# Kernel optimization log

Measured on AMD Instinct MI355X. Metric: run time of the kernel, lower is better.

The kernel has to match this reference:

```python
import jax, jax.numpy as jnp
import numpy as np

EPS_NORM = 1e-12  # F.normalize eps
EPS_BN = 1e-5     # BatchNorm eps


def setup_inputs() -> dict:
    key = jax.random.key(0)
    ks = jax.random.split(key, 8)
    B, N, P, d = 64, 4, 128, 256  # batch, subgraphs, patches/subgraph, feature_dim
    h = 256                        # hidden2[-1]
    C = 2                          # num_class
    totP = N * P                   # 512 == num_patches
    feat = totP * h                # readout size = 131072

    def w(k, shape, s=0.02):
        return jax.random.normal(k, shape, dtype=jnp.float32) * s

    return {
        "x": jax.random.normal(ks[0], (B, totP, d), dtype=jnp.float32),
        "edge_prior_mask": jax.random.uniform(ks[1], (P, P), dtype=jnp.float32),
        # stage1 GCN layers (Linear stored as [in, out])
        "W1": w(ks[2], (d, h)), "b1": jnp.zeros((h,), jnp.float32),
        "g1": jnp.ones((h,), jnp.float32), "be1": jnp.zeros((h,), jnp.float32),
        "W2": w(ks[3], (h, h)), "b2": jnp.zeros((h,), jnp.float32),
        "g2": jnp.ones((h,), jnp.float32), "be2": jnp.zeros((h,), jnp.float32),
        # mlp_causal
        "Wm1": w(ks[4], (feat, 128), 0.005), "bm1": jnp.zeros((128,), jnp.float32),
        "gm1": jnp.ones((128,), jnp.float32), "bem1": jnp.zeros((128,), jnp.float32),
        "Wm2": w(ks[5], (128, 64)), "bm2": jnp.zeros((64,), jnp.float32),
        "gm2": jnp.ones((64,), jnp.float32), "bem2": jnp.zeros((64,), jnp.float32),
        "Wm3": w(ks[6], (64, C)), "bm3": jnp.zeros((C,), jnp.float32),
    }


def reference(x, edge_prior_mask, W1, b1, g1, be1, W2, b2, g2, be2,
              Wm1, bm1, gm1, bem1, Wm2, bm2, gm2, bem2, Wm3, bm3):
    B, totP, d = x.shape
    P = edge_prior_mask.shape[0]
    N = totP // P

    # ---- dynamic edges: per-subgraph cosine similarity * prior mask ----
    xb = x.reshape(B, N, P, d)
    nrm = jnp.linalg.norm(xb, axis=-1, keepdims=True)
    xn = xb / jnp.maximum(nrm, EPS_NORM)
    sim = (jnp.einsum('bnpd,bnqd->bnpq', xn, xn) + 1.0) * 0.5  # [B,N,P,P]
    blocks = sim * edge_prior_mask[None, None]

    # block-diagonal assembly [B, totP, totP]
    edges = jnp.zeros((B, totP, totP), dtype=x.dtype)
    for i in range(N):
        edges = edges.at[:, i * P:(i + 1) * P, i * P:(i + 1) * P].set(blocks[:, i])
    eye = jnp.eye(totP, dtype=x.dtype)
    edges = edges * (1.0 - eye)  # zero the diagonal

    # ---- symmetric degree normalization with self loops ----
    A = edges + eye
    deg = A.sum(-1)  # [B, totP]
    dinv = jnp.where(deg > 0, 1.0 / jnp.sqrt(jnp.maximum(deg, EPS_NORM)), 0.0)
    An = dinv[:, :, None] * A * dinv[:, None, :]

    # ---- two GCN layers: bmm(An, X @ W + b) -> BN (over batch+nodes) -> relu ----
    def bn_relu(hh, g, b):
        m = hh.mean(axis=(0, 1), keepdims=True)
        v = hh.var(axis=(0, 1), keepdims=True)
        return jax.nn.relu(g * (hh - m) / jnp.sqrt(v + EPS_BN) + b)

    h1 = bn_relu(jnp.einsum('bpq,bqh->bph', An, x @ W1 + b1), g1, be1)
    h2 = bn_relu(jnp.einsum('bpq,bqh->bph', An, h1 @ W2 + b2), g2, be2)

    # ---- readout + MLP head (dropout = identity in eval) ----
    graph = h2.reshape(B, -1)

    def bn1d(z, g, b):
        m = z.mean(0, keepdims=True)
        v = z.var(0, keepdims=True)
        return g * (z - m) / jnp.sqrt(v + EPS_BN) + b

    z = jax.nn.relu(bn1d(graph @ Wm1 + bm1, gm1, bem1))
    z = jax.nn.relu(bn1d(z @ Wm2 + bm2, gm2, bem2))
    return z @ Wm3 + bm3
```

## Files before the change

### kernel.cpp

```cpp
#include <hip/hip_runtime.h>
#include <cstdint>
#include <cstddef>

#define P_    128
#define H_    256
#define FEAT_ 131072

__global__ __launch_bounds__(256) void k_simfused(
    const float* __restrict__ x, const float* __restrict__ mask,
    float* __restrict__ An) {
  __shared__ float Xs[16][128];
  __shared__ float red[128][17];
  __shared__ float diag_s[128];
  __shared__ float inv_s[128];
  __shared__ float dinv_s[128];
  const int blk = blockIdx.x;
  const int t = threadIdx.x;
  const int tp = t >> 4, tq = t & 15;
  const float* Xb = x + (size_t)blk * (128 * 256);

  float v[8][8];
  #pragma unroll
  for (int i = 0; i < 8; ++i)
    #pragma unroll
    for (int j = 0; j < 8; ++j) v[i][j] = 0.f;

  for (int kc = 0; kc < 16; ++kc) {
    __syncthreads();
    #pragma unroll
    for (int l = 0; l < 2; ++l) {
      const int f = t + 256 * l;
      const int row = f >> 2, k4 = (f & 3) * 4;
      const float4 x4 = *(const float4*)(Xb + (size_t)row * 256 + kc * 16 + k4);
      Xs[k4 + 0][row] = x4.x;
      Xs[k4 + 1][row] = x4.y;
      Xs[k4 + 2][row] = x4.z;
      Xs[k4 + 3][row] = x4.w;
    }
    __syncthreads();
    #pragma unroll
    for (int k = 0; k < 16; ++k) {
      const float4 a0 = *(const float4*)&Xs[k][tp * 8];
      const float4 a1 = *(const float4*)&Xs[k][tp * 8 + 4];
      const float4 b0 = *(const float4*)&Xs[k][tq * 8];
      const float4 b1 = *(const float4*)&Xs[k][tq * 8 + 4];
      const float a[8] = {a0.x, a0.y, a0.z, a0.w, a1.x, a1.y, a1.z, a1.w};
      const float b[8] = {b0.x, b0.y, b0.z, b0.w, b1.x, b1.y, b1.z, b1.w};
      #pragma unroll
      for (int i = 0; i < 8; ++i)
        #pragma unroll
        for (int j = 0; j < 8; ++j) v[i][j] += a[i] * b[j];
    }
  }

  if (tp == tq) {
    #pragma unroll
    for (int i = 0; i < 8; ++i) diag_s[tp * 8 + i] = v[i][i];
  }
  __syncthreads();
  if (t < 128) inv_s[t] = 1.0f / fmaxf(sqrtf(diag_s[t]), 1e-12f);
  __syncthreads();

  float ivq[8];
  #pragma unroll
  for (int j = 0; j < 8; ++j) ivq[j] = inv_s[tq * 8 + j];

  #pragma unroll
  for (int i = 0; i < 8; ++i) {
    const int r = tp * 8 + i;
    const float ivp = inv_s[r];
    const float4 m0 = *(const float4*)(mask + r * 128 + tq * 8);
    const float4 m1 = *(const float4*)(mask + r * 128 + tq * 8 + 4);
    const float mm[8] = {m0.x, m0.y, m0.z, m0.w, m1.x, m1.y, m1.z, m1.w};
    float s = 0.f;
    #pragma unroll
    for (int j = 0; j < 8; ++j) {
      const int c = tq * 8 + j;
      const float vv = (r == c) ? 0.0f
                                : (v[i][j] * ivp * ivq[j] + 1.0f) * 0.5f * mm[j];
      v[i][j] = vv;
      s += vv;
    }
    red[r][tq] = s;
  }
  __syncthreads();
  if (t < 128) {
    float sm = 0.f;
    #pragma unroll
    for (int u = 0; u < 16; ++u) sm += red[t][u];
    const float deg = 1.0f + sm;
    dinv_s[t] = (deg > 0.0f) ? rsqrtf(fmaxf(deg, 1e-12f)) : 0.0f;
  }
  __syncthreads();

  float dq[8];
  #pragma unroll
  for (int j = 0; j < 8; ++j) dq[j] = dinv_s[tq * 8 + j];
  float* Ab = An + (size_t)blk * 16384;
  #pragma unroll
  for (int i = 0; i < 8; ++i) {
    const int r = tp * 8 + i;
    const float dp = dinv_s[r];
    float o[8];
    #pragma unroll
    for (int j = 0; j < 8; ++j) {
      const int c = tq * 8 + j;
      o[j] = (r == c) ? dp * dq[j] : v[i][j] * dp * dq[j];
    }
    *(float4*)(Ab + (size_t)r * 128 + tq * 8)     = make_float4(o[0], o[1], o[2], o[3]);
    *(float4*)(Ab + (size_t)r * 128 + tq * 8 + 4) = make_float4(o[4], o[5], o[6], o[7]);
  }
}

__global__ __launch_bounds__(256) void k_gemm_t(
    const float* __restrict__ A, const float* __restrict__ W,
    const float* __restrict__ bias, float* __restrict__ out) {
  __shared__ float As[16][132];
  __shared__ float Ws[16][132];
  const int rb = blockIdx.x, cb = blockIdx.y;
  const int t = threadIdx.x, tp = t >> 4, tq = t & 15;
  const int m0 = rb * 128, c0 = cb * 128;

  float acc[8][8];
  #pragma unroll
  for (int j = 0; j < 8; ++j) {
    const int cj = (j < 4) ? (tq * 4 + j) : (64 + tq * 4 + (j - 4));
    const float bj = bias[c0 + cj];
    #pragma unroll
    for (int i = 0; i < 8; ++i) acc[i][j] = bj;
  }

  for (int kc = 0; kc < 16; ++kc) {
    __syncthreads();
    #pragma unroll
    for (int l = 0; l < 2; ++l) {
      const int f = t + 256 * l;
      const int row = f >> 2, k4 = (f & 3) * 4;
      const float4 a4 = *(const float4*)(A + (size_t)(m0 + row) * 256 + kc * 16 + k4);
      As[k4 + 0][row] = a4.x;
      As[k4 + 1][row] = a4.y;
      As[k4 + 2][row] = a4.z;
      As[k4 + 3][row] = a4.w;
    }
    #pragma unroll
    for (int l = 0; l < 2; ++l) {
      const int f = t + 256 * l;
      const int k = f >> 5, c4 = (f & 31) * 4;
      *(float4*)&Ws[k][c4] =
          *(const float4*)(W + (size_t)(kc * 16 + k) * 256 + c0 + c4);
    }
    __syncthreads();
    #pragma unroll
    for (int k = 0; k < 16; ++k) {
      const float4 a0 = *(const float4*)&As[k][tp * 4];
      const float4 a1 = *(const float4*)&As[k][64 + tp * 4];
      const float4 w0 = *(const float4*)&Ws[k][tq * 4];
      const float4 w1 = *(const float4*)&Ws[k][64 + tq * 4];
      const float a[8] = {a0.x, a0.y, a0.z, a0.w, a1.x, a1.y, a1.z, a1.w};
      const float w[8] = {w0.x, w0.y, w0.z, w0.w, w1.x, w1.y, w1.z, w1.w};
      #pragma unroll
      for (int i = 0; i < 8; ++i)
        #pragma unroll
        for (int j = 0; j < 8; ++j) acc[i][j] += a[i] * w[j];
    }
  }

  #pragma unroll
  for (int i = 0; i < 8; ++i) {
    const int ri = (i < 4) ? (tp * 4 + i) : (64 + tp * 4 + (i - 4));
    float* orow = out + (size_t)(m0 + ri) * 256 + c0;
    *(float4*)(orow + tq * 4)      = make_float4(acc[i][0], acc[i][1], acc[i][2], acc[i][3]);
    *(float4*)(orow + 64 + tq * 4) = make_float4(acc[i][4], acc[i][5], acc[i][6], acc[i][7]);
  }
}

__global__ __launch_bounds__(256) void k_gemmbn_t(
    const float* __restrict__ A, const float* __restrict__ scsh,
    const float* __restrict__ W, const float* __restrict__ bias,
    float* __restrict__ out) {
  __shared__ float As[16][132];
  __shared__ float Ws[16][132];
  const int rb = blockIdx.x, cb = blockIdx.y;
  const int t = threadIdx.x, tp = t >> 4, tq = t & 15;
  const int m0 = rb * 128, c0 = cb * 128;

  float acc[8][8];
  #pragma unroll
  for (int j = 0; j < 8; ++j) {
    const int cj = (j < 4) ? (tq * 4 + j) : (64 + tq * 4 + (j - 4));
    const float bj = bias[c0 + cj];
    #pragma unroll
    for (int i = 0; i < 8; ++i) acc[i][j] = bj;
  }

  for (int kc = 0; kc < 16; ++kc) {
    __syncthreads();
    #pragma unroll
    for (int l = 0; l < 2; ++l) {
      const int f = t + 256 * l;
      const int row = f >> 2, k4 = (f & 3) * 4;
      const int col = kc * 16 + k4;
      const float4 a4 = *(const float4*)(A + (size_t)(m0 + row) * 256 + col);
      const float4 sc = *(const float4*)(scsh + col);
      const float4 sh = *(const float4*)(scsh + 256 + col);
      As[k4 + 0][row] = fmaxf(a4.x * sc.x + sh.x, 0.0f);
      As[k4 + 1][row] = fmaxf(a4.y * sc.y + sh.y, 0.0f);
      As[k4 + 2][row] = fmaxf(a4.z * sc.z + sh.z, 0.0f);
      As[k4 + 3][row] = fmaxf(a4.w * sc.w + sh.w, 0.0f);
    }
    #pragma unroll
    for (int l = 0; l < 2; ++l) {
      const int f = t + 256 * l;
      const int k = f >> 5, c4 = (f & 31) * 4;
      *(float4*)&Ws[k][c4] =
          *(const float4*)(W + (size_t)(kc * 16 + k) * 256 + c0 + c4);
    }
    __syncthreads();
    #pragma unroll
    for (int k = 0; k < 16; ++k) {
      const float4 a0 = *(const float4*)&As[k][tp * 4];
      const float4 a1 = *(const float4*)&As[k][64 + tp * 4];
      const float4 w0 = *(const float4*)&Ws[k][tq * 4];
      const float4 w1 = *(const float4*)&Ws[k][64 + tq * 4];
      const float a[8] = {a0.x, a0.y, a0.z, a0.w, a1.x, a1.y, a1.z, a1.w};
      const float w[8] = {w0.x, w0.y, w0.z, w0.w, w1.x, w1.y, w1.z, w1.w};
      #pragma unroll
      for (int i = 0; i < 8; ++i)
        #pragma unroll
        for (int j = 0; j < 8; ++j) acc[i][j] += a[i] * w[j];
    }
  }

  #pragma unroll
  for (int i = 0; i < 8; ++i) {
    const int ri = (i < 4) ? (tp * 4 + i) : (64 + tp * 4 + (i - 4));
    float* orow = out + (size_t)(m0 + ri) * 256 + c0;
    *(float4*)(orow + tq * 4)      = make_float4(acc[i][0], acc[i][1], acc[i][2], acc[i][3]);
    *(float4*)(orow + 64 + tq * 4) = make_float4(acc[i][4], acc[i][5], acc[i][6], acc[i][7]);
  }
}

__global__ __launch_bounds__(256) void k_bmmst(
    const float* __restrict__ An, const float* __restrict__ XW,
    float* __restrict__ out, float* __restrict__ part) {
  __shared__ float As[16][132];
  __shared__ float Ws[16][132];
  __shared__ float rs[16][128];
  __shared__ float rq[16][128];
  const int blk = blockIdx.x, cb = blockIdx.y;
  const int t = threadIdx.x, tp = t >> 4, tq = t & 15;
  const float* Ab = An + (size_t)blk * 16384;
  const float* Xb = XW + (size_t)blk * (128 * 256);

  float acc[8][8];
  #pragma unroll
  for (int i = 0; i < 8; ++i)
    #pragma unroll
    for (int j = 0; j < 8; ++j) acc[i][j] = 0.f;

  for (int kc = 0; kc < 8; ++kc) {
    __syncthreads();
    #pragma unroll
    for (int l = 0; l < 2; ++l) {
      const int f = t + 256 * l;
      const int row = f >> 2, k4 = (f & 3) * 4;
      const float4 a4 = *(const float4*)(Ab + (size_t)row * 128 + kc * 16 + k4);
      As[k4 + 0][row] = a4.x;
      As[k4 + 1][row] = a4.y;
      As[k4 + 2][row] = a4.z;
      As[k4 + 3][row] = a4.w;
    }
    #pragma unroll
    for (int l = 0; l < 2; ++l) {
      const int f = t + 256 * l;
      const int k = f >> 5, c4 = (f & 31) * 4;
      *(float4*)&Ws[k][c4] =
          *(const float4*)(Xb + (size_t)(kc * 16 + k) * 256 + cb * 128 + c4);
    }
    __syncthreads();
    #pragma unroll
    for (int k = 0; k < 16; ++k) {
      const float4 a0 = *(const float4*)&As[k][tp * 4];
      const float4 a1 = *(const float4*)&As[k][64 + tp * 4];
      const float4 w0 = *(const float4*)&Ws[k][tq * 4];
      const float4 w1 = *(const float4*)&Ws[k][64 + tq * 4];
      const float a[8] = {a0.x, a0.y, a0.z, a0.w, a1.x, a1.y, a1.z, a1.w};
      const float w[8] = {w0.x, w0.y, w0.z, w0.w, w1.x, w1.y, w1.z, w1.w};
      #pragma unroll
      for (int i = 0; i < 8; ++i)
        #pragma unroll
        for (int j = 0; j < 8; ++j) acc[i][j] += a[i] * w[j];
    }
  }

  #pragma unroll
  for (int j = 0; j < 8; ++j) {
    const int col = (j < 4) ? (tq * 4 + j) : (64 + tq * 4 + (j - 4));
    float cs = 0.f, cq = 0.f;
    #pragma unroll
    for (int i = 0; i < 8; ++i) { cs += acc[i][j]; cq += acc[i][j] * acc[i][j]; }
    rs[tp][col] = cs;
    rq[tp][col] = cq;
  }
  __syncthreads();
  if (t < 128) {
    float s = 0.f, q = 0.f;
    #pragma unroll
    for (int u = 0; u < 16; ++u) { s += rs[u][t]; q += rq[u][t]; }
    const int base = (blk * 2 + cb) * 256;
    part[base + t]       = s;
    part[base + 128 + t] = q;
  }

  #pragma unroll
  for (int i = 0; i < 8; ++i) {
    const int ri = (i < 4) ? (tp * 4 + i) : (64 + tp * 4 + (i - 4));
    float* orow = out + (size_t)(blk * 128 + ri) * 256 + cb * 128;
    *(float4*)(orow + tq * 4)      = make_float4(acc[i][0], acc[i][1], acc[i][2], acc[i][3]);
    *(float4*)(orow + 64 + tq * 4) = make_float4(acc[i][4], acc[i][5], acc[i][6], acc[i][7]);
  }
}

__global__ __launch_bounds__(256) void k_bnscsh(
    const float* __restrict__ part, const float* __restrict__ g,
    const float* __restrict__ be, float* __restrict__ scsh) {
  __shared__ float ss[256], qq[256];
  const int c = blockIdx.x;
  const int cb = c >> 7, lc = c & 127;
  const int u = threadIdx.x;
  const float* pb = part + (size_t)(u * 2 + cb) * 256;
  ss[u] = pb[lc];
  qq[u] = pb[128 + lc];
  __syncthreads();
  for (int st = 128; st; st >>= 1) {
    if (u < st) { ss[u] += ss[u + st]; qq[u] += qq[u + st]; }
    __syncthreads();
  }
  if (u == 0) {
    const float m = ss[0] * (1.0f / 32768.0f);
    const float var = qq[0] * (1.0f / 32768.0f) - m * m;
    const float sc = g[c] * rsqrtf(var + 1e-5f);
    scsh[c] = sc;
    scsh[256 + c] = be[c] - m * sc;
  }
}

__global__ __launch_bounds__(256) void k_headgemm_v3(
    const float* __restrict__ pre2, const float* __restrict__ scsh,
    const float* __restrict__ Wm1, float* __restrict__ part) {
  __shared__ float graphS[64][128];
  const int t = threadIdx.x;
  const int bid = blockIdx.x;
  const int k0 = bid * 128;
  const int cbase = k0 & 255;

  #pragma unroll
  for (int l = 0; l < 8; ++l) {
    const int f = t + 256 * l;
    const int row = f >> 5, c4 = (f & 31) * 4;
    const float4 p = *(const float4*)(pre2 + (size_t)row * FEAT_ + k0 + c4);
    const float4 sc = *(const float4*)(scsh + cbase + c4);
    const float4 sh = *(const float4*)(scsh + 256 + cbase + c4);
    graphS[row][c4 + 0] = fmaxf(p.x * sc.x + sh.x, 0.0f);
    graphS[row][c4 + 1] = fmaxf(p.y * sc.y + sh.y, 0.0f);
    graphS[row][c4 + 2] = fmaxf(p.z * sc.z + sh.z, 0.0f);
    graphS[row][c4 + 3] = fmaxf(p.w * sc.w + sh.w, 0.0f);
  }
  __syncthreads();

  const int hg = t & 31;
  const int bg = t >> 5;
  float acc[8][4];
  #pragma unroll
  for (int i = 0; i < 8; ++i)
    #pragma unroll
    for (int j = 0; j < 4; ++j) acc[i][j] = 0.f;

  #pragma unroll 2
  for (int kk = 0; kk < 128; kk += 4) {
    const int k = k0 + kk;
    const float4 w0 = *(const float4*)(Wm1 + (size_t)(k + 0) * 128 + hg * 4);
    const float4 w1 = *(const float4*)(Wm1 + (size_t)(k + 1) * 128 + hg * 4);
    const float4 w2 = *(const float4*)(Wm1 + (size_t)(k + 2) * 128 + hg * 4);
    const float4 w3 = *(const float4*)(Wm1 + (size_t)(k + 3) * 128 + hg * 4);
    #pragma unroll
    for (int i = 0; i < 8; ++i) {
      const float4 a = *(const float4*)&graphS[bg * 8 + i][kk];
      acc[i][0] += a.x * w0.x; acc[i][1] += a.x * w0.y;
      acc[i][2] += a.x * w0.z; acc[i][3] += a.x * w0.w;
      acc[i][0] += a.y * w1.x; acc[i][1] += a.y * w1.y;
      acc[i][2] += a.y * w1.z; acc[i][3] += a.y * w1.w;
      acc[i][0] += a.z * w2.x; acc[i][1] += a.z * w2.y;
      acc[i][2] += a.z * w2.z; acc[i][3] += a.z * w2.w;
      acc[i][0] += a.w * w3.x; acc[i][1] += a.w * w3.y;
      acc[i][2] += a.w * w3.z; acc[i][3] += a.w * w3.w;
    }
  }

  float* pb = part + (size_t)bid * 8192;
  #pragma unroll
  for (int i = 0; i < 8; ++i)
    *(float4*)(pb + (bg * 8 + i) * 128 + hg * 4) =
        make_float4(acc[i][0], acc[i][1], acc[i][2], acc[i][3]);
}

__global__ __launch_bounds__(256) void k_headredA(
    const float* __restrict__ part, float* __restrict__ part2) {
  const int o = blockIdx.x * 256 + threadIdx.x;
  const int jg = blockIdx.y;
  const float* base = part + (size_t)jg * 128 * 8192;
  float s = 0.f;
  for (int j = 0; j < 128; ++j) s += base[(size_t)j * 8192 + o];
  part2[(size_t)jg * 8192 + o] = s;
}

__global__ __launch_bounds__(256) void k_headtail(
    const float* __restrict__ part2,
    const float* __restrict__ gm1, const float* __restrict__ bem1,
    const float* __restrict__ Wm2,
    const float* __restrict__ gm2, const float* __restrict__ bem2,
    const float* __restrict__ Wm3, const float* __restrict__ bm3,
    float* __restrict__ out) {
  __shared__ float zs[8192];
  __shared__ float wm2s[8192];
  __shared__ float zb2[4096];
  __shared__ float sc1[128], sh1[128], sc2[64], sh2[64];
  const int t = threadIdx.x;

  for (int o = t; o < 8192; o += 256) {
    float s = 0.f;
    #pragma unroll
    for (int jg = 0; jg < 8; ++jg) s += part2[(size_t)jg * 8192 + o];
    zs[o] = s;
  }
  for (int o = t; o < 8192; o += 256) wm2s[o] = Wm2[o];
  __syncthreads();

  if (t < 128) {
    float s = 0.f, q = 0.f;
    for (int b = 0; b < 64; ++b) { const float v = zs[b * 128 + t]; s += v; q += v * v; }
    const float m = s * (1.0f / 64.0f);
    const float var = q * (1.0f / 64.0f) - m * m;
    const float sc = gm1[t] * rsqrtf(var + 1e-5f);
    sc1[t] = sc; sh1[t] = bem1[t] - m * sc;
  }
  __syncthreads();
  for (int o = t; o < 8192; o += 256)
    zs[o] = fmaxf(zs[o] * sc1[o & 127] + sh1[o & 127], 0.0f);
  __syncthreads();

  {
    const int bq = t >> 4, jq = t & 15;
    float acc[4][4];
    #pragma unroll
    for (int bi = 0; bi < 4; ++bi)
      #pragma unroll
      for (int ji = 0; ji < 4; ++ji) acc[bi][ji] = 0.f;
    for (int k = 0; k < 128; ++k) {
      const float4 w4 = *(const float4*)&wm2s[k * 64 + jq * 4];
      const float wv[4] = {w4.x, w4.y, w4.z, w4.w};
      #pragma unroll
      for (int bi = 0; bi < 4; ++bi) {
        const float zv = zs[(bq * 4 + bi) * 128 + k];
        #pragma unroll
        for (int ji = 0; ji < 4; ++ji) acc[bi][ji] += zv * wv[ji];
      }
    }
    #pragma unroll
    for (int bi = 0; bi < 4; ++bi)
      #pragma unroll
      for (int ji = 0; ji < 4; ++ji)
        zb2[(bq * 4 + bi) * 64 + jq * 4 + ji] = acc[bi][ji];
  }
  __syncthreads();

  if (t < 64) {
    float s = 0.f, q = 0.f;
    for (int b = 0; b < 64; ++b) { const float v = zb2[b * 64 + t]; s += v; q += v * v; }
    const float m = s * (1.0f / 64.0f);
    const float var = q * (1.0f / 64.0f) - m * m;
    const float sc = gm2[t] * rsqrtf(var + 1e-5f);
    sc2[t] = sc; sh2[t] = bem2[t] - m * sc;
  }
  __syncthreads();
  for (int idx = t; idx < 4096; idx += 256)
    zb2[idx] = fmaxf(zb2[idx] * sc2[idx & 63] + sh2[idx & 63], 0.0f);
  __syncthreads();

  if (t < 128) {
    const int b = t >> 1, c = t & 1;
    float s = bm3[c];
    for (int k = 0; k < 64; ++k) s += zb2[b * 64 + k] * Wm3[k * 2 + c];
    out[t] = s;
  }
}

extern "C" void kernel_launch(void* const* d_in, const int* in_sizes, int n_in,
                              void* d_out, int out_size, void* d_ws, size_t ws_size,
                              hipStream_t stream) {
  (void)in_sizes; (void)n_in; (void)out_size; (void)ws_size;
  const float* x    = (const float*)d_in[0];
  const float* mask = (const float*)d_in[1];
  const float* W1   = (const float*)d_in[2];
  const float* b1   = (const float*)d_in[3];
  const float* g1   = (const float*)d_in[4];
  const float* be1  = (const float*)d_in[5];
  const float* W2   = (const float*)d_in[6];
  const float* b2   = (const float*)d_in[7];
  const float* g2   = (const float*)d_in[8];
  const float* be2  = (const float*)d_in[9];
  const float* Wm1  = (const float*)d_in[10];
  const float* gm1  = (const float*)d_in[12];
  const float* bem1 = (const float*)d_in[13];
  const float* Wm2  = (const float*)d_in[14];
  const float* gm2  = (const float*)d_in[16];
  const float* bem2 = (const float*)d_in[17];
  const float* Wm3  = (const float*)d_in[18];
  const float* bm3  = (const float*)d_in[19];

  float* ws   = (float*)d_ws;
  float* T1   = ws;
  float* An   = T1 + 8388608;
  float* T2   = An + 4194304;
  float* T3   = T2 + 8388608;
  float* z1   = T3 + 8388608;
  float* dinv = z1 + 8192;
  (void)z1;

  float* scsh1 = dinv;
  float* scsh2 = dinv + 512;

  k_simfused<<<256, 256, 0, stream>>>(x, mask, An);

  k_gemm_t<<<dim3(256, 2), 256, 0, stream>>>(x, W1, b1, T2);
  k_bmmst<<<dim3(256, 2), 256, 0, stream>>>(An, T2, T3, T1);
  k_bnscsh<<<256, 256, 0, stream>>>(T1, g1, be1, scsh1);

  k_gemmbn_t<<<dim3(256, 2), 256, 0, stream>>>(T3, scsh1, W2, b2, T2);
  k_bmmst<<<dim3(256, 2), 256, 0, stream>>>(An, T2, T3, T1);
  k_bnscsh<<<256, 256, 0, stream>>>(T1, g2, be2, scsh2);

  k_headgemm_v3<<<1024, 256, 0, stream>>>(T3, scsh2, Wm1, T2);
  k_headredA<<<dim3(32, 8), 256, 0, stream>>>(T2, An);
  k_headtail<<<1, 256, 0, stream>>>(An, gm1, bem1, Wm2, gm2, bem2,
                                    Wm3, bm3, (float*)d_out);
}
```

Measured before the change: 412.5 us.

## Split-K the first feature GEMM and double threads in similarity kernel

The first X@W1 GEMM is split into two K halves across a third grid dimension. Each half writes its own partial buffer, and the following batched An@XW kernel adds the two partials while loading its tile. The similarity/adjacency kernel now uses 512 threads per block, each computing 4x8 outputs instead of 8x8, to raise occupancy on a grid with only 256 blocks. The cost is an extra 32 MB partial write and read, plus a dropped restrict qualifier because the bmm input aliases its output buffer.

```diff
diff --git a/kernel.cpp b/kernel.cpp
--- a/kernel.cpp
+++ b/kernel.cpp
@@ -6,7 +6,7 @@
 #define H_    256
 #define FEAT_ 131072
 
-__global__ __launch_bounds__(256) void k_simfused(
+__global__ __launch_bounds__(512) void k_simfused(
     const float* __restrict__ x, const float* __restrict__ mask,
     float* __restrict__ An) {
   __shared__ float Xs[16][128];
@@ -19,18 +19,16 @@
   const int tp = t >> 4, tq = t & 15;
   const float* Xb = x + (size_t)blk * (128 * 256);
 
-  float v[8][8];
-  #pragma unroll
-  for (int i = 0; i < 8; ++i)
+  float v[4][8];
+  #pragma unroll
+  for (int i = 0; i < 4; ++i)
     #pragma unroll
     for (int j = 0; j < 8; ++j) v[i][j] = 0.f;
 
   for (int kc = 0; kc < 16; ++kc) {
     __syncthreads();
-    #pragma unroll
-    for (int l = 0; l < 2; ++l) {
-      const int f = t + 256 * l;
-      const int row = f >> 2, k4 = (f & 3) * 4;
+    {
+      const int row = t >> 2, k4 = (t & 3) * 4;
       const float4 x4 = *(const float4*)(Xb + (size_t)row * 256 + kc * 16 + k4);
       Xs[k4 + 0][row] = x4.x;
       Xs[k4 + 1][row] = x4.y;
@@ -40,22 +38,23 @@
     __syncthreads();
     #pragma unroll
     for (int k = 0; k < 16; ++k) {
-      const float4 a0 = *(const float4*)&Xs[k][tp * 8];
-      const float4 a1 = *(const float4*)&Xs[k][tp * 8 + 4];
+      const float4 a0 = *(const float4*)&Xs[k][tp * 4];
       const float4 b0 = *(const float4*)&Xs[k][tq * 8];
       const float4 b1 = *(const float4*)&Xs[k][tq * 8 + 4];
-      const float a[8] = {a0.x, a0.y, a0.z, a0.w, a1.x, a1.y, a1.z, a1.w};
+      const float a[4] = {a0.x, a0.y, a0.z, a0.w};
       const float b[8] = {b0.x, b0.y, b0.z, b0.w, b1.x, b1.y, b1.z, b1.w};
       #pragma unroll
-      for (int i = 0; i < 8; ++i)
+      for (int i = 0; i < 4; ++i)
         #pragma unroll
         for (int j = 0; j < 8; ++j) v[i][j] += a[i] * b[j];
     }
   }
 
-  if (tp == tq) {
-    #pragma unroll
-    for (int i = 0; i < 8; ++i) diag_s[tp * 8 + i] = v[i][i];
+  #pragma unroll
+  for (int i = 0; i < 4; ++i) {
+    const int r = tp * 4 + i;
+    const int jd = r - tq * 8;
+    if (jd >= 0 && jd < 8) diag_s[r] = v[i][jd];
   }
   __syncthreads();
   if (t < 128) inv_s[t] = 1.0f / fmaxf(sqrtf(diag_s[t]), 1e-12f);
@@ -66,8 +65,8 @@
   for (int j = 0; j < 8; ++j) ivq[j] = inv_s[tq * 8 + j];
 
   #pragma unroll
-  for (int i = 0; i < 8; ++i) {
-    const int r = tp * 8 + i;
+  for (int i = 0; i < 4; ++i) {
+    const int r = tp * 4 + i;
     const float ivp = inv_s[r];
     const float4 m0 = *(const float4*)(mask + r * 128 + tq * 8);
     const float4 m1 = *(const float4*)(mask + r * 128 + tq * 8 + 4);
@@ -98,8 +97,8 @@
   for (int j = 0; j < 8; ++j) dq[j] = dinv_s[tq * 8 + j];
   float* Ab = An + (size_t)blk * 16384;
   #pragma unroll
-  for (int i = 0; i < 8; ++i) {
-    const int r = tp * 8 + i;
+  for (int i = 0; i < 4; ++i) {
+    const int r = tp * 4 + i;
     const float dp = dinv_s[r];
     float o[8];
     #pragma unroll
@@ -114,29 +113,31 @@
 
 __global__ __launch_bounds__(256) void k_gemm_t(
     const float* __restrict__ A, const float* __restrict__ W,
-    const float* __restrict__ bias, float* __restrict__ out) {
+    const float* __restrict__ bias, float* __restrict__ out0,
+    float* __restrict__ out1) {
   __shared__ float As[16][132];
   __shared__ float Ws[16][132];
-  const int rb = blockIdx.x, cb = blockIdx.y;
+  const int rb = blockIdx.x, cb = blockIdx.y, kh = blockIdx.z;
   const int t = threadIdx.x, tp = t >> 4, tq = t & 15;
-  const int m0 = rb * 128, c0 = cb * 128;
+  const int m0 = rb * 128, c0 = cb * 128, kbase = kh * 128;
 
   float acc[8][8];
   #pragma unroll
   for (int j = 0; j < 8; ++j) {
     const int cj = (j < 4) ? (tq * 4 + j) : (64 + tq * 4 + (j - 4));
-    const float bj = bias[c0 + cj];
+    const float bj = (kh == 0) ? bias[c0 + cj] : 0.0f;
     #pragma unroll
     for (int i = 0; i < 8; ++i) acc[i][j] = bj;
   }
 
-  for (int kc = 0; kc < 16; ++kc) {
+  for (int kc = 0; kc < 8; ++kc) {
     __syncthreads();
     #pragma unroll
     for (int l = 0; l < 2; ++l) {
       const int f = t + 256 * l;
       const int row = f >> 2, k4 = (f & 3) * 4;
-      const float4 a4 = *(const float4*)(A + (size_t)(m0 + row) * 256 + kc * 16 + k4);
+      const float4 a4 = *(const float4*)(A + (size_t)(m0 + row) * 256 +
+                                         kbase + kc * 16 + k4);
       As[k4 + 0][row] = a4.x;
       As[k4 + 1][row] = a4.y;
       As[k4 + 2][row] = a4.z;
@@ -147,7 +148,7 @@
       const int f = t + 256 * l;
       const int k = f >> 5, c4 = (f & 31) * 4;
       *(float4*)&Ws[k][c4] =
-          *(const float4*)(W + (size_t)(kc * 16 + k) * 256 + c0 + c4);
+          *(const float4*)(W + (size_t)(kbase + kc * 16 + k) * 256 + c0 + c4);
     }
     __syncthreads();
     #pragma unroll
@@ -165,10 +166,11 @@
     }
   }
 
+  float* outp = kh ? out1 : out0;
   #pragma unroll
   for (int i = 0; i < 8; ++i) {
     const int ri = (i < 4) ? (tp * 4 + i) : (64 + tp * 4 + (i - 4));
-    float* orow = out + (size_t)(m0 + ri) * 256 + c0;
+    float* orow = outp + (size_t)(m0 + ri) * 256 + c0;
     *(float4*)(orow + tq * 4)      = make_float4(acc[i][0], acc[i][1], acc[i][2], acc[i][3]);
     *(float4*)(orow + 64 + tq * 4) = make_float4(acc[i][4], acc[i][5], acc[i][6], acc[i][7]);
   }
@@ -241,8 +243,8 @@
 }
 
 __global__ __launch_bounds__(256) void k_bmmst(
-    const float* __restrict__ An, const float* __restrict__ XW,
-    float* __restrict__ out, float* __restrict__ part) {
+    const float* __restrict__ An, const float* XW0, const float* XW1,
+    float* out, float* __restrict__ part) {
   __shared__ float As[16][132];
   __shared__ float Ws[16][132];
   __shared__ float rs[16][128];
@@ -250,7 +252,8 @@
   const int blk = blockIdx.x, cb = blockIdx.y;
   const int t = threadIdx.x, tp = t >> 4, tq = t & 15;
   const float* Ab = An + (size_t)blk * 16384;
-  const float* Xb = XW + (size_t)blk * (128 * 256);
+  const float* Xb0 = XW0 + (size_t)blk * (128 * 256);
+  const float* Xb1 = XW1 ? (XW1 + (size_t)blk * (128 * 256)) : nullptr;
 
   float acc[8][8];
   #pragma unroll
@@ -274,8 +277,13 @@
     for (int l = 0; l < 2; ++l) {
       const int f = t + 256 * l;
       const int k = f >> 5, c4 = (f & 31) * 4;
-      *(float4*)&Ws[k][c4] =
-          *(const float4*)(Xb + (size_t)(kc * 16 + k) * 256 + cb * 128 + c4);
+      const size_t idx = (size_t)(kc * 16 + k) * 256 + cb * 128 + c4;
+      float4 w4 = *(const float4*)(Xb0 + idx);
+      if (Xb1) {
+        const float4 w4b = *(const float4*)(Xb1 + idx);
+        w4.x += w4b.x; w4.y += w4b.y; w4.z += w4b.z; w4.w += w4b.w;
+      }
+      *(float4*)&Ws[k][c4] = w4;
     }
     __syncthreads();
     #pragma unroll
@@ -530,14 +538,14 @@
   float* scsh1 = dinv;
   float* scsh2 = dinv + 512;
 
-  k_simfused<<<256, 256, 0, stream>>>(x, mask, An);
-
-  k_gemm_t<<<dim3(256, 2), 256, 0, stream>>>(x, W1, b1, T2);
-  k_bmmst<<<dim3(256, 2), 256, 0, stream>>>(An, T2, T3, T1);
+  k_simfused<<<256, 512, 0, stream>>>(x, mask, An);
+
+  k_gemm_t<<<dim3(256, 2, 2), 256, 0, stream>>>(x, W1, b1, T2, T3);
+  k_bmmst<<<dim3(256, 2), 256, 0, stream>>>(An, T2, T3, T3, T1);
   k_bnscsh<<<256, 256, 0, stream>>>(T1, g1, be1, scsh1);
 
   k_gemmbn_t<<<dim3(256, 2), 256, 0, stream>>>(T3, scsh1, W2, b2, T2);
-  k_bmmst<<<dim3(256, 2), 256, 0, stream>>>(An, T2, T3, T1);
+  k_bmmst<<<dim3(256, 2), 256, 0, stream>>>(An, T2, nullptr, T3, T1);
   k_bnscsh<<<256, 256, 0, stream>>>(T1, g2, be2, scsh2);
 
   k_headgemm_v3<<<1024, 256, 0, stream>>>(T3, scsh2, Wm1, T2);
```

Result: no change. 419.2 us (+1.6%).

## Fuse per-layer feature GEMM and adjacency bmm into one kernel via shared memory

Applied to the files above, without the earlier changes.

Merges the X@W+b GEMM and the An@XW batched matmul (with BN partial stats) into a single k_layer kernel. The 128x128 XW tile stays in shared memory instead of round-tripping through global memory, and two launches per GCN layer are removed. In exchange, shared memory per block grows to about 84KB, which lowers occupancy, and the two GEMM phases run back to back with no overlap. Buffer assignments for the head kernels are swapped to match the new output locations.

```diff
diff --git a/kernel.cpp b/kernel.cpp
--- a/kernel.cpp
+++ b/kernel.cpp
@@ -112,77 +112,20 @@
   }
 }
 
-__global__ __launch_bounds__(256) void k_gemm_t(
-    const float* __restrict__ A, const float* __restrict__ W,
-    const float* __restrict__ bias, float* __restrict__ out) {
-  __shared__ float As[16][132];
-  __shared__ float Ws[16][132];
-  const int rb = blockIdx.x, cb = blockIdx.y;
+#define XW_OFF 0
+#define ST_OFF 16896
+#define SW_OFF 19008
+#define RS_OFF 16896
+#define RQ_OFF 18944
+
+__global__ __launch_bounds__(256) void k_layer(
+    const float* __restrict__ An, const float* X, const float* scsh,
+    const float* __restrict__ W, const float* __restrict__ bias,
+    float* out, float* __restrict__ part) {
+  __shared__ float smem[21120];
+  const int blk = blockIdx.x, cb = blockIdx.y;
   const int t = threadIdx.x, tp = t >> 4, tq = t & 15;
-  const int m0 = rb * 128, c0 = cb * 128;
-
-  float acc[8][8];
-  #pragma unroll
-  for (int j = 0; j < 8; ++j) {
-    const int cj = (j < 4) ? (tq * 4 + j) : (64 + tq * 4 + (j - 4));
-    const float bj = bias[c0 + cj];
-    #pragma unroll
-    for (int i = 0; i < 8; ++i) acc[i][j] = bj;
-  }
-
-  for (int kc = 0; kc < 16; ++kc) {
-    __syncthreads();
-    #pragma unroll
-    for (int l = 0; l < 2; ++l) {
-      const int f = t + 256 * l;
-      const int row = f >> 2, k4 = (f & 3) * 4;
-      const float4 a4 = *(const float4*)(A + (size_t)(m0 + row) * 256 + kc * 16 + k4);
-      As[k4 + 0][row] = a4.x;
-      As[k4 + 1][row] = a4.y;
-      As[k4 + 2][row] = a4.z;
-      As[k4 + 3][row] = a4.w;
-    }
-    #pragma unroll
-    for (int l = 0; l < 2; ++l) {
-      const int f = t + 256 * l;
-      const int k = f >> 5, c4 = (f & 31) * 4;
-      *(float4*)&Ws[k][c4] =
-          *(const float4*)(W + (size_t)(kc * 16 + k) * 256 + c0 + c4);
-    }
-    __syncthreads();
-    #pragma unroll
-    for (int k = 0; k < 16; ++k) {
-      const float4 a0 = *(const float4*)&As[k][tp * 4];
-      const float4 a1 = *(const float4*)&As[k][64 + tp * 4];
-      const float4 w0 = *(const float4*)&Ws[k][tq * 4];
-      const float4 w1 = *(const float4*)&Ws[k][64 + tq * 4];
-      const float a[8] = {a0.x, a0.y, a0.z, a0.w, a1.x, a1.y, a1.z, a1.w};
-      const float w[8] = {w0.x, w0.y, w0.z, w0.w, w1.x, w1.y, w1.z, w1.w};
-      #pragma unroll
-      for (int i = 0; i < 8; ++i)
-        #pragma unroll
-        for (int j = 0; j < 8; ++j) acc[i][j] += a[i] * w[j];
-    }
-  }
-
-  #pragma unroll
-  for (int i = 0; i < 8; ++i) {
-    const int ri = (i < 4) ? (tp * 4 + i) : (64 + tp * 4 + (i - 4));
-    float* orow = out + (size_t)(m0 + ri) * 256 + c0;
-    *(float4*)(orow + tq * 4)      = make_float4(acc[i][0], acc[i][1], acc[i][2], acc[i][3]);
-    *(float4*)(orow + 64 + tq * 4) = make_float4(acc[i][4], acc[i][5], acc[i][6], acc[i][7]);
-  }
-}
-
-__global__ __launch_bounds__(256) void k_gemmbn_t(
-    const float* __restrict__ A, const float* __restrict__ scsh,
-    const float* __restrict__ W, const float* __restrict__ bias,
-    float* __restrict__ out) {
-  __shared__ float As[16][132];
-  __shared__ float Ws[16][132];
-  const int rb = blockIdx.x, cb = blockIdx.y;
-  const int t = threadIdx.x, tp = t >> 4, tq = t & 15;
-  const int m0 = rb * 128, c0 = cb * 128;
+  const int m0 = blk * 128, c0 = cb * 128;
 
   float acc[8][8];
   #pragma unroll
@@ -200,28 +143,34 @@
       const int f = t + 256 * l;
       const int row = f >> 2, k4 = (f & 3) * 4;
       const int col = kc * 16 + k4;
-      const float4 a4 = *(const float4*)(A + (size_t)(m0 + row) * 256 + col);
-      const float4 sc = *(const float4*)(scsh + col);
-      const float4 sh = *(const float4*)(scsh + 256 + col);
-      As[k4 + 0][row] = fmaxf(a4.x * sc.x + sh.x, 0.0f);
-      As[k4 + 1][row] = fmaxf(a4.y * sc.y + sh.y, 0.0f);
-      As[k4 + 2][row] = fmaxf(a4.z * sc.z + sh.z, 0.0f);
-      As[k4 + 3][row] = fmaxf(a4.w * sc.w + sh.w, 0.0f);
+      float4 a4 = *(const float4*)(X + (size_t)(m0 + row) * 256 + col);
+      if (scsh) {
+        const float4 sc = *(const float4*)(scsh + col);
+        const float4 sh = *(const float4*)(scsh + 256 + col);
+        a4.x = fmaxf(a4.x * sc.x + sh.x, 0.0f);
+        a4.y = fmaxf(a4.y * sc.y + sh.y, 0.0f);
+        a4.z = fmaxf(a4.z * sc.z + sh.z, 0.0f);
+        a4.w = fmaxf(a4.w * sc.w + sh.w, 0.0f);
+      }
+      smem[ST_OFF + (k4 + 0) * 132 + row] = a4.x;
+      smem[ST_OFF + (k4 + 1) * 132 + row] = a4.y;
+      smem[ST_OFF + (k4 + 2) * 132 + row] = a4.z;
+      smem[ST_OFF + (k4 + 3) * 132 + row] = a4.w;
     }
     #pragma unroll
     for (int l = 0; l < 2; ++l) {
       const int f = t + 256 * l;
       const int k = f >> 5, c4 = (f & 31) * 4;
-      *(float4*)&Ws[k][c4] =
+      *(float4*)&smem[SW_OFF + k * 132 + c4] =
           *(const float4*)(W + (size_t)(kc * 16 + k) * 256 + c0 + c4);
     }
     __syncthreads();
     #pragma unroll
     for (int k = 0; k < 16; ++k) {
-      const float4 a0 = *(const float4*)&As[k][tp * 4];
-      const float4 a1 = *(const float4*)&As[k][64 + tp * 4];
-      const float4 w0 = *(const float4*)&Ws[k][tq * 4];
-      const float4 w1 = *(const float4*)&Ws[k][64 + tq * 4];
+      const float4 a0 = *(const float4*)&smem[ST_OFF + k * 132 + tp * 4];
+      const float4 a1 = *(const float4*)&smem[ST_OFF + k * 132 + 64 + tp * 4];
+      const float4 w0 = *(const float4*)&smem[SW_OFF + k * 132 + tq * 4];
+      const float4 w1 = *(const float4*)&smem[SW_OFF + k * 132 + 64 + tq * 4];
       const float a[8] = {a0.x, a0.y, a0.z, a0.w, a1.x, a1.y, a1.z, a1.w};
       const float w[8] = {w0.x, w0.y, w0.z, w0.w, w1.x, w1.y, w1.z, w1.w};
       #pragma unroll
@@ -231,33 +180,24 @@
     }
   }
 
+  __syncthreads();
   #pragma unroll
   for (int i = 0; i < 8; ++i) {
     const int ri = (i < 4) ? (tp * 4 + i) : (64 + tp * 4 + (i - 4));
-    float* orow = out + (size_t)(m0 + ri) * 256 + c0;
-    *(float4*)(orow + tq * 4)      = make_float4(acc[i][0], acc[i][1], acc[i][2], acc[i][3]);
-    *(float4*)(orow + 64 + tq * 4) = make_float4(acc[i][4], acc[i][5], acc[i][6], acc[i][7]);
-  }
-}
-
-__global__ __launch_bounds__(256) void k_bmmst(
-    const float* __restrict__ An, const float* __restrict__ XW,
-    float* __restrict__ out, float* __restrict__ part) {
-  __shared__ float As[16][132];
-  __shared__ float Ws[16][132];
-  __shared__ float rs[16][128];
-  __shared__ float rq[16][128];
-  const int blk = blockIdx.x, cb = blockIdx.y;
-  const int t = threadIdx.x, tp = t >> 4, tq = t & 15;
+    *(float4*)&smem[XW_OFF + ri * 132 + tq * 4] =
+        make_float4(acc[i][0], acc[i][1], acc[i][2], acc[i][3]);
+    *(float4*)&smem[XW_OFF + ri * 132 + 64 + tq * 4] =
+        make_float4(acc[i][4], acc[i][5], acc[i][6], acc[i][7]);
+  }
+  __syncthreads();
+
+  float acc2[8][8];
+  #pragma unroll
+  for (int i = 0; i < 8; ++i)
+    #pragma unroll
+    for (int j = 0; j < 8; ++j) acc2[i][j] = 0.f;
+
   const float* Ab = An + (size_t)blk * 16384;
-  const float* Xb = XW + (size_t)blk * (128 * 256);
-
-  float acc[8][8];
-  #pragma unroll
-  for (int i = 0; i < 8; ++i)
-    #pragma unroll
-    for (int j = 0; j < 8; ++j) acc[i][j] = 0.f;
-
   for (int kc = 0; kc < 8; ++kc) {
     __syncthreads();
     #pragma unroll
@@ -265,48 +205,46 @@
       const int f = t + 256 * l;
       const int row = f >> 2, k4 = (f & 3) * 4;
       const float4 a4 = *(const float4*)(Ab + (size_t)row * 128 + kc * 16 + k4);
-      As[k4 + 0][row] = a4.x;
-      As[k4 + 1][row] = a4.y;
-      As[k4 + 2][row] = a4.z;
-      As[k4 + 3][row] = a4.w;
-    }
-    #pragma unroll
-    for (int l = 0; l < 2; ++l) {
-      const int f = t + 256 * l;
-      const int k = f >> 5, c4 = (f & 31) * 4;
-      *(float4*)&Ws[k][c4] =
-          *(const float4*)(Xb + (size_t)(kc * 16 + k) * 256 + cb * 128 + c4);
+      smem[ST_OFF + (k4 + 0) * 132 + row] = a4.x;
+      smem[ST_OFF + (k4 + 1) * 132 + row] = a4.y;
+      smem[ST_OFF + (k4 + 2) * 132 + row] = a4.z;
+      smem[ST_OFF + (k4 + 3) * 132 + row] = a4.w;
     }
     __syncthreads();
     #pragma unroll
     for (int k = 0; k < 16; ++k) {
-      const float4 a0 = *(const float4*)&As[k][tp * 4];
-      const float4 a1 = *(const float4*)&As[k][64 + tp * 4];
-      const float4 w0 = *(const float4*)&Ws[k][tq * 4];
-      const float4 w1 = *(const float4*)&Ws[k][64 + tq * 4];
+      const int q = kc * 16 + k;
+      const float4 a0 = *(const float4*)&smem[ST_OFF + k * 132 + tp * 4];
+      const float4 a1 = *(const float4*)&smem[ST_OFF + k * 132 + 64 + tp * 4];
+      const float4 w0 = *(const float4*)&smem[XW_OFF + q * 132 + tq * 4];
+      const float4 w1 = *(const float4*)&smem[XW_OFF + q * 132 + 64 + tq * 4];
       const float a[8] = {a0.x, a0.y, a0.z, a0.w, a1.x, a1.y, a1.z, a1.w};
       const float w[8] = {w0.x, w0.y, w0.z, w0.w, w1.x, w1.y, w1.z, w1.w};
       #pragma unroll
       for (int i = 0; i < 8; ++i)
         #pragma unroll
-        for (int j = 0; j < 8; ++j) acc[i][j] += a[i] * w[j];
-    }
-  }
-
+        for (int j = 0; j < 8; ++j) acc2[i][j] += a[i] * w[j];
+    }
+  }
+
+  __syncthreads();
   #pragma unroll
   for (int j = 0; j < 8; ++j) {
     const int col = (j < 4) ? (tq * 4 + j) : (64 + tq * 4 + (j - 4));
     float cs = 0.f, cq = 0.f;
     #pragma unroll
-    for (int i = 0; i < 8; ++i) { cs += acc[i][j]; cq += acc[i][j] * acc[i][j]; }
-    rs[tp][col] = cs;
-    rq[tp][col] = cq;
+    for (int i = 0; i < 8; ++i) { cs += acc2[i][j]; cq += acc2[i][j] * acc2[i][j]; }
+    smem[RS_OFF + tp * 128 + col] = cs;
+    smem[RQ_OFF + tp * 128 + col] = cq;
   }
   __syncthreads();
   if (t < 128) {
     float s = 0.f, q = 0.f;
     #pragma unroll
-    for (int u = 0; u < 16; ++u) { s += rs[u][t]; q += rq[u][t]; }
+    for (int u = 0; u < 16; ++u) {
+      s += smem[RS_OFF + u * 128 + t];
+      q += smem[RQ_OFF + u * 128 + t];
+    }
     const int base = (blk * 2 + cb) * 256;
     part[base + t]       = s;
     part[base + 128 + t] = q;
@@ -315,9 +253,9 @@
   #pragma unroll
   for (int i = 0; i < 8; ++i) {
     const int ri = (i < 4) ? (tp * 4 + i) : (64 + tp * 4 + (i - 4));
-    float* orow = out + (size_t)(blk * 128 + ri) * 256 + cb * 128;
-    *(float4*)(orow + tq * 4)      = make_float4(acc[i][0], acc[i][1], acc[i][2], acc[i][3]);
-    *(float4*)(orow + 64 + tq * 4) = make_float4(acc[i][4], acc[i][5], acc[i][6], acc[i][7]);
+    float* orow = out + (size_t)(m0 + ri) * 256 + c0;
+    *(float4*)(orow + tq * 4)      = make_float4(acc2[i][0], acc2[i][1], acc2[i][2], acc2[i][3]);
+    *(float4*)(orow + 64 + tq * 4) = make_float4(acc2[i][4], acc2[i][5], acc2[i][6], acc2[i][7]);
   }
 }
 
@@ -532,16 +470,14 @@
 
   k_simfused<<<256, 256, 0, stream>>>(x, mask, An);
 
-  k_gemm_t<<<dim3(256, 2), 256, 0, stream>>>(x, W1, b1, T2);
-  k_bmmst<<<dim3(256, 2), 256, 0, stream>>>(An, T2, T3, T1);
+  k_layer<<<dim3(256, 2), 256, 0, stream>>>(An, x, nullptr, W1, b1, T3, T1);
   k_bnscsh<<<256, 256, 0, stream>>>(T1, g1, be1, scsh1);
 
-  k_gemmbn_t<<<dim3(256, 2), 256, 0, stream>>>(T3, scsh1, W2, b2, T2);
-  k_bmmst<<<dim3(256, 2), 256, 0, stream>>>(An, T2, T3, T1);
+  k_layer<<<dim3(256, 2), 256, 0, stream>>>(An, T3, scsh1, W2, b2, T2, T1);
   k_bnscsh<<<256, 256, 0, stream>>>(T1, g2, be2, scsh2);
 
-  k_headgemm_v3<<<1024, 256, 0, stream>>>(T3, scsh2, Wm1, T2);
-  k_headredA<<<dim3(32, 8), 256, 0, stream>>>(T2, An);
+  k_headgemm_v3<<<1024, 256, 0, stream>>>(T2, scsh2, Wm1, T3);
+  k_headredA<<<dim3(32, 8), 256, 0, stream>>>(T3, An);
   k_headtail<<<1, 256, 0, stream>>>(An, gm1, bem1, Wm2, gm2, bem2,
                                     Wm3, bm3, (float*)d_out);
 }
```

New measurement: 479.1 us. 1.16x slower.
